# Performance work log

Hardware: AMD Instinct MI355X
Metric: run time of the kernel (lower is better)

Reference implementation:

```python
import jax, jax.numpy as jnp
import numpy as np

B, F, V, D = 4096, 8, 1000, 1024  # batch, n_fields, vocab per field, hidden_size
LN_EPS = 1e-5


def layer_norm(x, g, b, eps=LN_EPS):
    mu = x.mean(axis=-1, keepdims=True)
    var = ((x - mu) ** 2).mean(axis=-1, keepdims=True)
    return (x - mu) * jax.lax.rsqrt(var + eps) * g + b


def setup_inputs() -> dict:
    key = jax.random.key(0)
    k0, k1, k2, k3 = jax.random.split(key, 4)
    return {
        "input_embedding": jax.random.normal(k0, (B, D), jnp.float32),
        "features": jax.random.randint(k1, (B, F), 0, V),
        "embed_tables": jax.random.normal(k2, (F, V, D), jnp.float32) * 0.02,
        "ln_gamma": jnp.ones((D,), jnp.float32),
        "ln_beta": jnp.zeros((D,), jnp.float32),
        "pred_W": jax.random.normal(k3, (F, D, V), jnpp := jnp.float32) * 0.02,
        "pred_b": jnp.zeros((F, V), jnp.float32),
    }


def reference(input_embedding, features, embed_tables, ln_gamma, ln_beta, pred_W, pred_b):
    # Per-field embedding lookup: (B, F, D)
    feat_emb = embed_tables[jnp.arange(F)[None, :], features]
    # Stack input embedding first, as in torch.stack([input_embedding] + ...):
    embeddings = jnp.concatenate([input_embedding[:, None, :], feat_emb], axis=1)  # (B, F+1, D)
    # triu(diagonal=1) masked broadcast-sum then [:, 1:, :] == exclusive causal prefix sum:
    # masked_sums[:, j] = sum_{i < j+1} embeddings[:, i] for j = 0..F-1
    masked_sums = jnp.cumsum(embeddings, axis=1)[:, :F, :]  # (B, F, D)
    h = jax.nn.gelu(layer_norm(masked_sums, ln_gamma, ln_beta), approximate=False)
    # Per-field predictor heads (Linear(D, V)), batched over fields:
    logits = jnp.einsum("bfd,fdv->bfv", h, pred_W) + pred_b  # (B, F, V)
    return logits
```

## Files before the change

kernel.cpp:

```cpp
#include <hip/hip_runtime.h>
#include <hip/hip_bf16.h>

#define B_ 4096
#define F_ 8
#define V_ 1000
#define D_ 1024
#define VP 1024

typedef __bf16 bf16x8 __attribute__((ext_vector_type(8)));
typedef float f32x4 __attribute__((ext_vector_type(4)));

__device__ __forceinline__ void gload_lds16(const void* g, void* l) {
  __builtin_amdgcn_global_load_lds(
      (const __attribute__((address_space(1))) void*)g,
      (__attribute__((address_space(3))) void*)l, 16, 0, 0);
}

__global__ __launch_bounds__(256) void transpose_w(
    const float* __restrict__ W, __hip_bfloat16* __restrict__ Wt) {
  __shared__ float tile[32][33];
  const int f = blockIdx.z;
  const int k0 = blockIdx.x * 32;
  const int v0 = blockIdx.y * 32;
  const int tx = threadIdx.x;
  const int ty = threadIdx.y;
  const float* Wf = W + (size_t)f * D_ * V_;
#pragma unroll
  for (int i = 0; i < 4; ++i) {
    int k = k0 + ty + i * 8;
    int v = v0 + tx;
    tile[ty + i * 8][tx] = (v < V_) ? Wf[k * V_ + v] : 0.0f;
  }
  __syncthreads();
  __hip_bfloat16* Wtf = Wt + (size_t)f * VP * D_;
#pragma unroll
  for (int i = 0; i < 4; ++i) {
    int v = v0 + ty + i * 8;
    int k = k0 + tx;
    Wtf[v * D_ + k] = __float2bfloat16(tile[tx][ty + i * 8]);
  }
}

__global__ __launch_bounds__(256) void fuse_h(
    const float* __restrict__ emb, const int* __restrict__ feats,
    const float* __restrict__ tables, const float* __restrict__ gamma,
    const float* __restrict__ beta, __hip_bfloat16* __restrict__ H) {
  const int b = blockIdx.x;
  const int t = threadIdx.x;
  const int d = t * 4;
  const int wave = t >> 6, lane = t & 63;

  float s[4];
  {
    float4 v = *reinterpret_cast<const float4*>(&emb[(size_t)b * D_ + d]);
    s[0] = v.x; s[1] = v.y; s[2] = v.z; s[3] = v.w;
  }
  float gm[4], bt[4];
  {
    float4 g = *reinterpret_cast<const float4*>(&gamma[d]);
    float4 bb = *reinterpret_cast<const float4*>(&beta[d]);
    gm[0] = g.x; gm[1] = g.y; gm[2] = g.z; gm[3] = g.w;
    bt[0] = bb.x; bt[1] = bb.y; bt[2] = bb.z; bt[3] = bb.w;
  }
  __shared__ float red[2][4][2];

  for (int f = 0; f < F_; ++f) {
    float sum = s[0] + s[1] + s[2] + s[3];
    float ssq = s[0] * s[0] + s[1] * s[1] + s[2] * s[2] + s[3] * s[3];
#pragma unroll
    for (int off = 32; off > 0; off >>= 1) {
      sum += __shfl_xor(sum, off, 64);
      ssq += __shfl_xor(ssq, off, 64);
    }
    const int pb = f & 1;
    if (lane == 0) { red[pb][wave][0] = sum; red[pb][wave][1] = ssq; }
    __syncthreads();
    sum = red[pb][0][0] + red[pb][1][0] + red[pb][2][0] + red[pb][3][0];
    ssq = red[pb][0][1] + red[pb][1][1] + red[pb][2][1] + red[pb][3][1];

    const float mu = sum * (1.0f / D_);
    const float var = ssq * (1.0f / D_) - mu * mu;
    const float rstd = rsqrtf(var + 1e-5f);

    __hip_bfloat16 hb[4];
#pragma unroll
    for (int j = 0; j < 4; ++j) {
      float x = (s[j] - mu) * rstd * gm[j] + bt[j];
      float g = 0.5f * x * (1.0f + erff(x * 0.70710678118654752f));
      hb[j] = __float2bfloat16(g);
    }
    *reinterpret_cast<uint2*>(&H[(size_t)f * (B_ * D_) + (size_t)b * D_ + d]) =
        *reinterpret_cast<const uint2*>(hb);

    if (f < F_ - 1) {
      int feat = feats[b * F_ + f];
      const float* row = tables + ((size_t)f * V_ + feat) * D_;
      float4 tv = *reinterpret_cast<const float4*>(&row[d]);
      s[0] += tv.x; s[1] += tv.y; s[2] += tv.z; s[3] += tv.w;
    }
  }
}

#define AOFF 0
#define BOFF 32768

#define STAGE(OPB, GB, DBUF, HALF, KT)                                        \
  do {                                                                        \
    const ushort* _g = (GB) + (size_t)(HALF) * (128 * D_) + (size_t)(KT) * 64;\
    ushort* _l = &lds[(OPB) + ((DBUF)*2 + (HALF)) * 8192 + w * 512];          \
    gload_lds16(_g, _l);                                                      \
    gload_lds16(_g + 64 * D_, _l + 4096);                                     \
  } while (0)

#define LD_A(DST, LBASE, FIOFF)                                               \
  _Pragma("unroll") for (int _fj = 0; _fj < 4; ++_fj)                         \
  _Pragma("unroll") for (int _ks = 0; _ks < 2; ++_ks)                         \
      DST[_fj][_ks] = *reinterpret_cast<const bf16x8*>(                       \
          (LBASE) + ((((FIOFF) + _fj) * 2 + _ks) * 512));

#define LD_B(DST, LBASE, NFOFF)                                               \
  _Pragma("unroll") for (int _fn = 0; _fn < 2; ++_fn)                         \
  _Pragma("unroll") for (int _ks = 0; _ks < 2; ++_ks)                         \
      DST[_fn][_ks] = *reinterpret_cast<const bf16x8*>(                       \
          (LBASE) + ((((NFOFF) + _fn) * 2 + _ks) * 512));

#define Q_MFMA(AF, BF, R0, C0)                                                \
  do {                                                                        \
    __builtin_amdgcn_s_setprio(1);                                            \
    _Pragma("unroll") for (int _fj = 0; _fj < 4; ++_fj)                       \
    _Pragma("unroll") for (int _fn = 0; _fn < 2; ++_fn)                       \
    _Pragma("unroll") for (int _ks = 0; _ks < 2; ++_ks)                       \
        acc[(R0) + _fj][(C0) + _fn] =                                         \
            __builtin_amdgcn_mfma_f32_16x16x32_bf16(                          \
                AF[_fj][_ks], BF[_fn][_ks], acc[(R0) + _fj][(C0) + _fn],      \
                0, 0, 0);                                                     \
    __builtin_amdgcn_s_setprio(0);                                            \
  } while (0)

#define PHB                                                                   \
  do {                                                                        \
    asm volatile("" ::: "memory");                                            \
    __builtin_amdgcn_s_barrier();                                             \
    asm volatile("" ::: "memory");                                            \
  } while (0)

#define SB0 __builtin_amdgcn_sched_barrier(0)
#define WAITV6 asm volatile("s_waitcnt vmcnt(6)" ::: "memory")
#define WAITV0 asm volatile("s_waitcnt vmcnt(0)" ::: "memory")

__global__ __launch_bounds__(512, 2) void gemm_hw(
    const ushort* __restrict__ H,
    const ushort* __restrict__ Wt,
    const float* __restrict__ bias,
    float* __restrict__ out) {
  __shared__ ushort lds[65536];

  const int bid = blockIdx.x;
  const int swz = (bid & 7) * 64 + (bid >> 3);
  const int f = swz >> 6;
  const int r = swz & 63;
  const int mt = r >> 2, nt = r & 3;

  const int t = threadIdx.x;
  const int w = t >> 6, l = t & 63;
  const int wm = w >> 2;
  const int wn = w & 3;

  const ushort* Hf = H + (size_t)f * (B_ * D_);
  const ushort* Wf = Wt + (size_t)f * (VP * D_);

  const int srow = ((w >> 1) << 4) + (l >> 2);
  const int skx = ((w & 1) << 5) + ((((l & 3) << 3)) ^ (((l >> 5) & 1) << 4));
  const ushort* gA = Hf + (size_t)(mt * 256 + srow) * D_ + skx;
  const ushort* gB = Wf + (size_t)(nt * 256 + srow) * D_ + skx;

  const int laneu =
      ((l & 15) << 5) + (((((l >> 4) << 4)) ^ (((l >> 3) & 1) << 5)) >> 1);
  const ushort* lA[2] = {&lds[(0 * 2 + wm) * 8192 + laneu],
                         &lds[(1 * 2 + wm) * 8192 + laneu]};
  const ushort* lB[2] = {
      &lds[BOFF + (0 * 2 + (wn >> 1)) * 8192 + (wn & 1) * 4096 + laneu],
      &lds[BOFF + (1 * 2 + (wn >> 1)) * 8192 + (wn & 1) * 4096 + laneu]};

  bf16x8 a0[4][2], a1[4][2], b0[2][2], b1[2][2];
  f32x4 acc[8][4] = {};

  STAGE(AOFF, gA, 0, 0, 0);
  STAGE(AOFF, gA, 0, 1, 0);
  STAGE(BOFF, gB, 0, 0, 0);
  STAGE(BOFF, gB, 0, 1, 0);
  STAGE(AOFF, gA, 1, 0, 1);
  STAGE(AOFF, gA, 1, 1, 1);
  STAGE(BOFF, gB, 1, 0, 1);
  WAITV6;
  PHB;
  LD_A(a0, lA[0], 0);
  LD_B(b0, lB[0], 0);
  SB0;

#pragma unroll 1
  for (int i = 0; i < 8; ++i) {
    const int t1 = 2 * i + 1, t2 = 2 * i + 2, t3 = 2 * i + 3;
    const bool more = (i < 7);
    STAGE(BOFF, gB, 1, 1, t1);
    PHB;
    LD_A(a1, lA[0], 4);
    SB0;
    Q_MFMA(a0, b0, 0, 0);
    if (more) STAGE(AOFF, gA, 0, 0, t2);
    PHB;
    LD_B(b1, lB[0], 2);
    SB0;
    Q_MFMA(a1, b0, 4, 0);
    if (more) STAGE(AOFF, gA, 0, 1, t2);
    PHB;
    SB0;
    Q_MFMA(a0, b1, 0, 2);
    if (more) STAGE(BOFF, gB, 0, 0, t2);
    if (more) { WAITV6; } else { WAITV0; }
    PHB;
    LD_A(a0, lA[1], 0);
    LD_B(b0, lB[1], 0);
    SB0;
    Q_MFMA(a1, b1, 4, 2);
    if (more) STAGE(BOFF, gB, 0, 1, t2);
    PHB;
    LD_A(a1, lA[1], 4);
    SB0;
    Q_MFMA(a0, b0, 0, 0);
    if (more) STAGE(AOFF, gA, 1, 0, t3);
    PHB;
    LD_B(b1, lB[1], 2);
    SB0;
    Q_MFMA(a1, b0, 4, 0);
    if (more) STAGE(AOFF, gA, 1, 1, t3);
    PHB;
    SB0;
    Q_MFMA(a0, b1, 0, 2);
    if (more) {
      STAGE(BOFF, gB, 1, 0, t3);
      WAITV6;
    }
    PHB;
    if (more) {
      LD_A(a0, lA[0], 0);
      LD_B(b0, lB[0], 0);
    }
    SB0;
    Q_MFMA(a1, b1, 4, 2);
  }

  const float* bp = bias + f * V_;
  const int orow0 = mt * 256 + wm * 128 + ((l >> 4) << 2);
  const int ocol0 = nt * 256 + wn * 64 + (l & 15);
#pragma unroll
  for (int fi = 0; fi < 8; ++fi) {
#pragma unroll
    for (int fn = 0; fn < 4; ++fn) {
      int col = ocol0 + fn * 16;
      if (col < V_) {
        float bb = bp[col];
        int row = orow0 + fi * 16;
        float* op = out + (size_t)row * (F_ * V_) + (size_t)f * V_ + col;
#pragma unroll
        for (int q = 0; q < 4; ++q)
          op[(size_t)q * (F_ * V_)] = acc[fi][fn][q] + bb;
      }
    }
  }
}

extern "C" void kernel_launch(void* const* d_in, const int* in_sizes, int n_in,
                              void* d_out, int out_size, void* d_ws,
                              size_t ws_size, hipStream_t stream) {
  const float* emb = (const float*)d_in[0];
  const int* feats = (const int*)d_in[1];
  const float* tables = (const float*)d_in[2];
  const float* gamma = (const float*)d_in[3];
  const float* beta = (const float*)d_in[4];
  const float* W = (const float*)d_in[5];
  const float* bias = (const float*)d_in[6];
  float* out = (float*)d_out;

  char* ws = (char*)d_ws;
  __hip_bfloat16* Hbuf = (__hip_bfloat16*)ws;
  __hip_bfloat16* Wtbuf =
      (__hip_bfloat16*)(ws + (size_t)F_ * B_ * D_ * 2);

  transpose_w<<<dim3(D_ / 32, VP / 32, F_), dim3(32, 8), 0, stream>>>(W, Wtbuf);
  fuse_h<<<dim3(B_), dim3(256), 0, stream>>>(emb, feats, tables, gamma, beta,
                                             Hbuf);
  gemm_hw<<<dim3((B_ / 256) * (VP / 256) * F_), dim3(512), 0, stream>>>(
      (const ushort*)Hbuf, (const ushort*)Wtbuf, bias, out);
}
```

Before: 135.7 us.

## Restructure GEMM main loop schedule with explicit lgkmcnt waits and reordered staging

Reorders the phases of the GEMM main loop so the LDS fragment reads are issued before the barrier and global stage loads, with explicit lgkmcnt(0) waits replacing compiler memory fences. The global-to-LDS stage for B tile 1 part 0 moves into the loop, and the vmcnt threshold changes from 6 to 4 to match the new number of outstanding loads. The aim is better overlap of LDS reads and global prefetch with MFMA work. Dropping the memory clobbers and moving staging relative to barriers risks read/write races on the LDS buffers if the wait counts are wrong.

```diff
diff --git a/kernel.cpp b/kernel.cpp
--- a/kernel.cpp
+++ b/kernel.cpp
@@ -137,16 +137,11 @@
     __builtin_amdgcn_s_setprio(0);                                            \
   } while (0)
 
-#define PHB                                                                   \
-  do {                                                                        \
-    asm volatile("" ::: "memory");                                            \
-    __builtin_amdgcn_s_barrier();                                             \
-    asm volatile("" ::: "memory");                                            \
-  } while (0)
-
+#define BAR __builtin_amdgcn_s_barrier()
 #define SB0 __builtin_amdgcn_sched_barrier(0)
-#define WAITV6 asm volatile("s_waitcnt vmcnt(6)" ::: "memory")
-#define WAITV0 asm volatile("s_waitcnt vmcnt(0)" ::: "memory")
+#define VM4 asm volatile("s_waitcnt vmcnt(4)")
+#define VM0 asm volatile("s_waitcnt vmcnt(0)")
+#define LG0 asm volatile("s_waitcnt lgkmcnt(0)")
 
 __global__ __launch_bounds__(512, 2) void gemm_hw(
     const ushort* __restrict__ H,
@@ -191,61 +186,65 @@
   STAGE(BOFF, gB, 0, 1, 0);
   STAGE(AOFF, gA, 1, 0, 1);
   STAGE(AOFF, gA, 1, 1, 1);
-  STAGE(BOFF, gB, 1, 0, 1);
-  WAITV6;
-  PHB;
-  LD_A(a0, lA[0], 0);
-  LD_B(b0, lB[0], 0);
-  SB0;
+  VM4;
+  BAR;
 
 #pragma unroll 1
   for (int i = 0; i < 8; ++i) {
     const int t1 = 2 * i + 1, t2 = 2 * i + 2, t3 = 2 * i + 3;
     const bool more = (i < 7);
+    LD_A(a0, lA[0], 0);
+    LD_B(b0, lB[0], 0);
+    STAGE(BOFF, gB, 1, 0, t1);
+    BAR;
+    LG0;
+    SB0;
+    Q_MFMA(a0, b0, 0, 0);
+    LD_A(a1, lA[0], 4);
     STAGE(BOFF, gB, 1, 1, t1);
-    PHB;
-    LD_A(a1, lA[0], 4);
-    SB0;
-    Q_MFMA(a0, b0, 0, 0);
+    BAR;
+    LG0;
+    SB0;
+    Q_MFMA(a1, b0, 4, 0);
+    LD_B(b1, lB[0], 2);
     if (more) STAGE(AOFF, gA, 0, 0, t2);
-    PHB;
-    LD_B(b1, lB[0], 2);
-    SB0;
-    Q_MFMA(a1, b0, 4, 0);
-    if (more) STAGE(AOFF, gA, 0, 1, t2);
-    PHB;
+    BAR;
+    LG0;
     SB0;
     Q_MFMA(a0, b1, 0, 2);
-    if (more) STAGE(BOFF, gB, 0, 0, t2);
-    if (more) { WAITV6; } else { WAITV0; }
-    PHB;
+    if (more) {
+      STAGE(AOFF, gA, 0, 1, t2);
+      VM4;
+    } else {
+      VM0;
+    }
+    BAR;
+    SB0;
+    Q_MFMA(a1, b1, 4, 2);
     LD_A(a0, lA[1], 0);
     LD_B(b0, lB[1], 0);
-    SB0;
-    Q_MFMA(a1, b1, 4, 2);
+    if (more) STAGE(BOFF, gB, 0, 0, t2);
+    BAR;
+    LG0;
+    SB0;
+    Q_MFMA(a0, b0, 0, 0);
+    LD_A(a1, lA[1], 4);
     if (more) STAGE(BOFF, gB, 0, 1, t2);
-    PHB;
-    LD_A(a1, lA[1], 4);
-    SB0;
-    Q_MFMA(a0, b0, 0, 0);
+    BAR;
+    LG0;
+    SB0;
+    Q_MFMA(a1, b0, 4, 0);
+    LD_B(b1, lB[1], 2);
     if (more) STAGE(AOFF, gA, 1, 0, t3);
-    PHB;
-    LD_B(b1, lB[1], 2);
-    SB0;
-    Q_MFMA(a1, b0, 4, 0);
-    if (more) STAGE(AOFF, gA, 1, 1, t3);
-    PHB;
+    BAR;
+    LG0;
     SB0;
     Q_MFMA(a0, b1, 0, 2);
     if (more) {
-      STAGE(BOFF, gB, 1, 0, t3);
-      WAITV6;
-    }
-    PHB;
-    if (more) {
-      LD_A(a0, lA[0], 0);
-      LD_B(b0, lB[0], 0);
-    }
+      STAGE(AOFF, gA, 1, 1, t3);
+      VM4;
+    }
+    BAR;
     SB0;
     Q_MFMA(a1, b1, 4, 2);
   }
```

Measured after the change: 134.5 us. Within noise of the previous version (-0.9%).
